# Kernel tuning notes

Hardware: AMD Instinct MI355X
Metric: run time of the kernel (lower is better)

Reference implementation:

```python
import jax, jax.numpy as jnp
import numpy as np

T, D, DFF, E, K, CAP = 8192, 1024, 4096, 8, 2, 2560


def setup_inputs() -> dict:
    key = jax.random.key(0)
    ks = jax.random.split(key, 6)
    return {
        "x_flat": jax.random.normal(ks[0], (T, D), dtype=jnp.float32),
        "idx_flat": jax.random.randint(ks[1], (T, K), 0, E, dtype=jnp.int32),
        "scores_flat": jax.random.uniform(ks[2], (T, K), dtype=jnp.float32),
        "capacity": CAP,
        "W1": jax.random.normal(ks[3], (E, D, DFF), dtype=jnp.float32) * 0.02,
        "B1": jnp.zeros((E, DFF), dtype=jnp.float32),
        "W2": jax.random.normal(ks[4], (E, DFF, D), dtype=jnp.float32) * 0.02,
        "B2": jnp.zeros((E, D), dtype=jnp.float32),
    }


def reference(x_flat, idx_flat, scores_flat, capacity, W1, B1, W2, B2):
    # Fused MoE dispatch: capacity-limited gather -> per-expert FFN (grouped GEMM)
    # -> weighted scatter-combine.
    Ttok, d = x_flat.shape
    k = idx_flat.shape[1]
    e = idx_flat.reshape(-1)                      # [T*k] expert id per assignment
    s = scores_flat.reshape(-1)                   # [T*k] gate score
    tok = jnp.repeat(jnp.arange(Ttok), k)         # [T*k] source token index

    oh = jax.nn.one_hot(e, W1.shape[0], dtype=jnp.int32)   # [T*k, E]
    # slot of each assignment within its expert (0-based arrival order)
    pos = jnp.sum(jnp.cumsum(oh, axis=0) * oh, axis=1) - 1  # [T*k]
    keep = pos < capacity                                   # drop overflow tokens
    pos_c = jnp.where(keep, pos, 0)

    # gather tokens into per-expert buffers [E, capacity, d]
    xe = jnp.zeros((W1.shape[0], capacity, d), dtype=x_flat.dtype)
    xe = xe.at[e, pos_c].add(jnp.where(keep[:, None], x_flat[tok], 0.0))

    # per-expert FFN (grouped GEMM)
    h = jax.nn.gelu(jnp.einsum('ecd,edf->ecf', xe, W1) + B1[:, None, :])
    y = jnp.einsum('ecf,efd->ecd', h, W2) + B2[:, None, :]   # [E, capacity, d]

    # scatter back, scaled by gate scores
    yg = y[e, pos_c] * (s * keep.astype(s.dtype))[:, None]   # [T*k, d]
    out = jnp.zeros_like(x_flat).at[tok].add(yg)
    return out
```

## Files before the change

kernel.cpp:

```cpp
#include <hip/hip_runtime.h>
#include <hip/hip_bf16.h>

#define T_TOK   8192
#define D_MODEL 1024
#define DFF     4096
#define N_EXP   8
#define TOPK    2
#define CAP     2560
#define NASSIGN (T_TOK * TOPK)

typedef unsigned short u16;
typedef __attribute__((ext_vector_type(8))) short  short8;
typedef __attribute__((ext_vector_type(8))) unsigned short u16x8;
typedef __attribute__((ext_vector_type(4))) float  f32x4;


__device__ inline u16 f2bf(float f) {
    union { float f; unsigned u; } v; v.f = f;
    unsigned u = v.u;
    unsigned r = (u + 0x7fffu + ((u >> 16) & 1u)) >> 16;
    return (u16)r;
}

__device__ inline float gelu_tanh(float x) {
    float z = 0.7978845608028654f * (x + 0.044715f * x * x * x);
    z = fminf(fmaxf(z, -15.f), 15.f);
    float ez = __expf(2.f * z);
    float t = (ez - 1.f) / (ez + 1.f);
    return 0.5f * x * (1.f + t);
}

__device__ inline void gload_lds16(const void* g, void* l) {
    __builtin_amdgcn_global_load_lds(
        (const __attribute__((address_space(1))) unsigned int*)g,
        (__attribute__((address_space(3))) unsigned int*)l, 16, 0, 0);
}

__global__ __launch_bounds__(256) void scan_kernel(
    const int* __restrict__ idx, int* __restrict__ counts,
    int* __restrict__ pos_arr, int* __restrict__ slot_src)
{
    const int eb = blockIdx.x;
    const int tid = threadIdx.x;
    __shared__ int sbuf[256];
    const int CHUNK = NASSIGN / 256;
    const int base_i = tid * CHUNK;
    int local = 0;
    #pragma unroll 8
    for (int j = 0; j < CHUNK; ++j) local += (idx[base_i + j] == eb) ? 1 : 0;
    sbuf[tid] = local;
    __syncthreads();
    for (int off = 1; off < 256; off <<= 1) {
        int v = (tid >= off) ? sbuf[tid - off] : 0;
        __syncthreads();
        sbuf[tid] += v;
        __syncthreads();
    }
    int run = sbuf[tid] - local;
    for (int j = 0; j < CHUNK; ++j) {
        int i = base_i + j;
        if (idx[i] == eb) {
            if (run < CAP) { pos_arr[i] = run; slot_src[eb * CAP + run] = i / TOPK; }
            else           { pos_arr[i] = -1; }
            ++run;
        }
    }
    if (tid == 0) {
        int tot = sbuf[255];
        counts[eb] = tot < CAP ? tot : CAP;
    }
}

__global__ __launch_bounds__(256) void transpose_cvt(
    const float* __restrict__ in, u16* __restrict__ out, int R, int C)
{
    __shared__ float tile[32][33];
    const int e = blockIdx.z;
    const int c0 = blockIdx.x * 32, r0 = blockIdx.y * 32;
    const float* ine = in + (size_t)e * R * C;
    u16* oute = out + (size_t)e * R * C;
    const int tx = threadIdx.x, ty = threadIdx.y;
    #pragma unroll
    for (int i = 0; i < 4; ++i) {
        int r = ty + i * 8;
        tile[r][tx] = ine[(size_t)(r0 + r) * C + c0 + tx];
    }
    __syncthreads();
    #pragma unroll
    for (int i = 0; i < 4; ++i) {
        int cr = ty + i * 8;
        oute[(size_t)(c0 + cr) * R + r0 + tx] = f2bf(tile[tx][cr]);
    }
}

__global__ __launch_bounds__(128) void gather_kernel(
    const float* __restrict__ x, const int* __restrict__ counts,
    const int* __restrict__ slot_src, u16* __restrict__ Xe)
{
    const int b = blockIdx.x;
    const int e = b / CAP, slot = b % CAP;
    const int tid = threadIdx.x;
    u16* dst = Xe + ((size_t)e * CAP + slot) * D_MODEL + tid * 8;
    if (slot < counts[e]) {
        const int tok = slot_src[b];
        const float4* src = (const float4*)(x + (size_t)tok * D_MODEL) + tid * 2;
        float4 a = src[0], c = src[1];
        u16x8 v;
        v[0] = f2bf(a.x); v[1] = f2bf(a.y); v[2] = f2bf(a.z); v[3] = f2bf(a.w);
        v[4] = f2bf(c.x); v[5] = f2bf(c.y); v[6] = f2bf(c.z); v[7] = f2bf(c.w);
        *(u16x8*)dst = v;
    } else {
        float4 z = {0.f, 0.f, 0.f, 0.f};
        *(float4*)dst = z;
    }
}

template<int KD, int ND, bool FUSE_GELU>
__global__ __launch_bounds__(256) void gemm_bt(
    const u16* __restrict__ A, const u16* __restrict__ Bt,
    const float* __restrict__ bias, void* __restrict__ Cout,
    const int* __restrict__ counts)
{
    const int e = blockIdx.z;
    const int brow = blockIdx.x * 128;
    if (brow >= counts[e]) return;
    const int bcol = blockIdx.y * 128;

    const char* Ae = (const char*)(A + (size_t)e * CAP * KD + (size_t)brow * KD);
    const char* Be = (const char*)(Bt + (size_t)e * ND * KD + (size_t)bcol * KD);

    __shared__ __align__(16) u16 lsA[128 * 32];
    __shared__ __align__(16) u16 lsB[128 * 32];

    const int tid = threadIdx.x;
    const int lane = tid & 63;
    const int w = tid >> 6;
    const int wr = (w >> 1) * 64, wc = (w & 1) * 64;
    const int lr = lane & 15, lq = lane >> 4;

    f32x4 acc[4][4] = {};

    const size_t rstride = (size_t)KD * 2;
    const char* ga0 = Ae + (size_t)(tid >> 2) * rstride + (size_t)(tid & 3) * 16;
    const char* gb0 = Be + (size_t)(tid >> 2) * rstride + (size_t)(tid & 3) * 16;
    char* la = (char*)lsA + tid * 16;
    char* lb = (char*)lsB + tid * 16;
    const size_t half = 64 * rstride;

    for (int kt = 0; kt < KD / 32; ++kt) {
        const size_t ko = (size_t)kt * 64;
        gload_lds16(ga0 + ko,        la);
        gload_lds16(ga0 + ko + half, la + 4096);
        gload_lds16(gb0 + ko,        lb);
        gload_lds16(gb0 + ko + half, lb + 4096);
        __syncthreads();
        short8 af[4], bfr[4];
        #pragma unroll
        for (int m = 0; m < 4; ++m)
            af[m] = *(const short8*)((const char*)lsA + ((wr + m * 16 + lr) * 64 + lq * 16));
        #pragma unroll
        for (int n = 0; n < 4; ++n)
            bfr[n] = *(const short8*)((const char*)lsB + ((wc + n * 16 + lr) * 64 + lq * 16));
        #pragma unroll
        for (int m = 0; m < 4; ++m)
            #pragma unroll
            for (int n = 0; n < 4; ++n)
                acc[m][n] = __builtin_amdgcn_mfma_f32_16x16x32_bf16(af[m], bfr[n], acc[m][n], 0, 0, 0);
        __syncthreads();
    }

    const float* be = bias + (size_t)e * ND + bcol;
    if (FUSE_GELU) {
        u16* Ce = (u16*)Cout + (size_t)e * CAP * ND + (size_t)brow * ND + bcol;
        #pragma unroll
        for (int m = 0; m < 4; ++m)
            #pragma unroll
            for (int n = 0; n < 4; ++n) {
                f32x4 v = acc[m][n];
                int c = wc + n * 16 + lr;
                float bb = be[c];
                #pragma unroll
                for (int j = 0; j < 4; ++j) {
                    int r = wr + m * 16 + lq * 4 + j;
                    Ce[(size_t)r * ND + c] = f2bf(gelu_tanh(v[j] + bb));
                }
            }
    } else {
        float* Ce = (float*)Cout + (size_t)e * CAP * ND + (size_t)brow * ND + bcol;
        #pragma unroll
        for (int m = 0; m < 4; ++m)
            #pragma unroll
            for (int n = 0; n < 4; ++n) {
                f32x4 v = acc[m][n];
                int c = wc + n * 16 + lr;
                float bb = be[c];
                #pragma unroll
                for (int j = 0; j < 4; ++j) {
                    int r = wr + m * 16 + lq * 4 + j;
                    Ce[(size_t)r * ND + c] = v[j] + bb;
                }
            }
    }
}

__global__ __launch_bounds__(256) void scatter_kernel(
    const int* __restrict__ idx, const float* __restrict__ scores,
    const int* __restrict__ pos_arr, const float* __restrict__ Y,
    float* __restrict__ out)
{
    const int t = blockIdx.x;
    const int tid = threadIdx.x;
    float4 acc = {0.f, 0.f, 0.f, 0.f};
    #pragma unroll
    for (int k = 0; k < TOPK; ++k) {
        int i = t * TOPK + k;
        int p = pos_arr[i];
        if (p >= 0) {
            int e = idx[i];
            float s = scores[i];
            float4 v = *(const float4*)(Y + ((size_t)e * CAP + p) * D_MODEL + tid * 4);
            acc.x += s * v.x; acc.y += s * v.y; acc.z += s * v.z; acc.w += s * v.w;
        }
    }
    *(float4*)(out + (size_t)t * D_MODEL + tid * 4) = acc;
}

extern "C" void kernel_launch(void* const* d_in, const int* in_sizes, int n_in,
                              void* d_out, int out_size, void* d_ws, size_t ws_size,
                              hipStream_t stream)
{
    const float* x      = (const float*)d_in[0];
    const int*   idx    = (const int*)d_in[1];
    const float* scores = (const float*)d_in[2];
    const float* W1 = (const float*)d_in[4];
    const float* B1 = (const float*)d_in[5];
    const float* W2 = (const float*)d_in[6];
    const float* B2 = (const float*)d_in[7];
    float* out = (float*)d_out;

    char* ws = (char*)d_ws;
    size_t off = 0;
    auto alloc = [&](size_t bytes) {
        char* p = ws + off;
        off += (bytes + 255) & ~(size_t)255;
        return p;
    };
    int* counts   = (int*)alloc(N_EXP * 4);
    int* pos_arr  = (int*)alloc((size_t)NASSIGN * 4);
    int* slot_src = (int*)alloc((size_t)N_EXP * CAP * 4);
    u16* W1b = (u16*)alloc((size_t)N_EXP * D_MODEL * DFF * 2);
    u16* Xe  = (u16*)alloc((size_t)N_EXP * CAP * D_MODEL * 2);
    u16* W2b = (u16*)alloc((size_t)N_EXP * DFF * D_MODEL * 2);
    u16* H   = (u16*)alloc((size_t)N_EXP * CAP * DFF * 2);
    float* Y = (float*)W1b;

    scan_kernel<<<N_EXP, 256, 0, stream>>>(idx, counts, pos_arr, slot_src);
    transpose_cvt<<<dim3(DFF / 32, D_MODEL / 32, N_EXP), dim3(32, 8), 0, stream>>>(
        W1, W1b, D_MODEL, DFF);
    transpose_cvt<<<dim3(D_MODEL / 32, DFF / 32, N_EXP), dim3(32, 8), 0, stream>>>(
        W2, W2b, DFF, D_MODEL);
    gather_kernel<<<N_EXP * CAP, 128, 0, stream>>>(x, counts, slot_src, Xe);
    gemm_bt<D_MODEL, DFF, true><<<dim3(CAP / 128, DFF / 128, N_EXP), 256, 0, stream>>>(
        Xe, W1b, B1, H, counts);
    gemm_bt<DFF, D_MODEL, false><<<dim3(CAP / 128, D_MODEL / 128, N_EXP), 256, 0, stream>>>(
        H, W2b, B2, Y, counts);
    scatter_kernel<<<T_TOK, 256, 0, stream>>>(idx, scores, pos_arr, Y, out);
}
```

Baseline: 830.1 us.

## Rewrite grouped GEMM as 256x256 tile, 8-wave, double-buffered swizzled LDS pipeline

Replaces the 128x128 single-buffered bf16 GEMM with a 256x256-tile, 512-thread kernel. It stages 64-wide K slices into 128KB of double-buffered LDS using XOR-swizzled async global-to-LDS loads, and interleaves prefetch of the next slices with MFMA groups under explicit barriers and vmcnt waits. It also remaps the flattened block id so neighbouring blocks are spread across XCDs, and it raises MFMA priority. The aim is to hide memory latency, cut LDS bank conflicts and raise arithmetic intensity, at the cost of large LDS use, high register pressure and hand-tuned waitcnt logic.

```diff
diff --git a/kernel.cpp b/kernel.cpp
--- a/kernel.cpp
+++ b/kernel.cpp
@@ -34,6 +34,14 @@
     __builtin_amdgcn_global_load_lds(
         (const __attribute__((address_space(1))) unsigned int*)g,
         (__attribute__((address_space(3))) unsigned int*)l, 16, 0, 0);
+}
+
+__device__ __forceinline__ void BARm() {
+    asm volatile("" ::: "memory");
+    __builtin_amdgcn_sched_barrier(0);
+    __builtin_amdgcn_s_barrier();
+    __builtin_amdgcn_sched_barrier(0);
+    asm volatile("" ::: "memory");
 }
 
 __global__ __launch_bounds__(256) void scan_kernel(
@@ -116,91 +124,146 @@
 }
 
 template<int KD, int ND, bool FUSE_GELU>
-__global__ __launch_bounds__(256) void gemm_bt(
+__global__ __launch_bounds__(512, 2) void gemm8(
     const u16* __restrict__ A, const u16* __restrict__ Bt,
     const float* __restrict__ bias, void* __restrict__ Cout,
-    const int* __restrict__ counts)
-{
-    const int e = blockIdx.z;
-    const int brow = blockIdx.x * 128;
+    const int* __restrict__ counts, int nx, int ny)
+{
+    __shared__ __align__(16) char lds[131072];
+
+    const int nwg = nx * ny * N_EXP;
+    const int cpx = nwg >> 3;
+    const int id2 = (blockIdx.x & 7) * cpx + (blockIdx.x >> 3);
+    const int e   = id2 / (nx * ny);
+    const int rem = id2 % (nx * ny);
+    const int bx = rem % nx, by = rem / nx;
+    const int brow = bx << 8;
     if (brow >= counts[e]) return;
-    const int bcol = blockIdx.y * 128;
-
-    const char* Ae = (const char*)(A + (size_t)e * CAP * KD + (size_t)brow * KD);
-    const char* Be = (const char*)(Bt + (size_t)e * ND * KD + (size_t)bcol * KD);
-
-    __shared__ __align__(16) u16 lsA[128 * 32];
-    __shared__ __align__(16) u16 lsB[128 * 32];
+    const int bcol = by << 8;
 
     const int tid = threadIdx.x;
+    const char* Ae = (const char*)(A + ((size_t)e * CAP + brow) * KD);
+    const char* Be = (const char*)(Bt + ((size_t)e * ND + bcol) * KD);
+    constexpr int RB = KD * 2;
+    constexpr int NT = KD / 64;
+
     const int lane = tid & 63;
-    const int w = tid >> 6;
-    const int wr = (w >> 1) * 64, wc = (w & 1) * 64;
+    const int wid = tid >> 6;
+    const int wm = wid >> 2, wn = wid & 3;
     const int lr = lane & 15, lq = lane >> 4;
 
-    f32x4 acc[4][4] = {};
-
-    const size_t rstride = (size_t)KD * 2;
-    const char* ga0 = Ae + (size_t)(tid >> 2) * rstride + (size_t)(tid & 3) * 16;
-    const char* gb0 = Be + (size_t)(tid >> 2) * rstride + (size_t)(tid & 3) * 16;
-    char* la = (char*)lsA + tid * 16;
-    char* lb = (char*)lsB + tid * 16;
-    const size_t half = 64 * rstride;
-
-    for (int kt = 0; kt < KD / 32; ++kt) {
-        const size_t ko = (size_t)kt * 64;
-        gload_lds16(ga0 + ko,        la);
-        gload_lds16(ga0 + ko + half, la + 4096);
-        gload_lds16(gb0 + ko,        lb);
-        gload_lds16(gb0 + ko + half, lb + 4096);
-        __syncthreads();
-        short8 af[4], bfr[4];
-        #pragma unroll
-        for (int m = 0; m < 4; ++m)
-            af[m] = *(const short8*)((const char*)lsA + ((wr + m * 16 + lr) * 64 + lq * 16));
-        #pragma unroll
-        for (int n = 0; n < 4; ++n)
-            bfr[n] = *(const short8*)((const char*)lsB + ((wc + n * 16 + lr) * 64 + lq * 16));
-        #pragma unroll
-        for (int m = 0; m < 4; ++m)
-            #pragma unroll
-            for (int n = 0; n < 4; ++n)
-                acc[m][n] = __builtin_amdgcn_mfma_f32_16x16x32_bf16(af[m], bfr[n], acc[m][n], 0, 0, 0);
-        __syncthreads();
+    const int srow0 = tid >> 2, ss = tid & 3;
+
+    #define STG(gbase, buf, slot, kb) do {                                         \
+        { int row_ = srow0;       int sl_ = ss ^ ((row_ >> 1) & 3);                \
+          gload_lds16((gbase) + (size_t)row_ * RB + (kb) + sl_ * 16,               \
+                      lds + (buf) * 65536 + (slot) * 16384 + tid * 16); }          \
+        { int row_ = 128 + srow0; int sl_ = ss ^ ((row_ >> 1) & 3);                \
+          gload_lds16((gbase) + (size_t)row_ * RB + (kb) + sl_ * 16,               \
+                      lds + (buf) * 65536 + (slot) * 16384 + 8192 + tid * 16); }   \
+    } while (0)
+
+    auto RD = [&](int buf, int slot, int row) -> short8 {
+        int sl = lq ^ ((row >> 1) & 3);
+        return *(const short8*)(lds + buf * 65536 + slot * 16384 + row * 64 + sl * 16);
+    };
+
+    f32x4 acc[8][4] = {};
+    short8 af[4], bf[4];
+
+    #define MFMA16(MB) do {                                                        \
+        __builtin_amdgcn_s_setprio(1);                                             \
+        _Pragma("unroll")                                                          \
+        for (int m_ = 0; m_ < 4; ++m_)                                             \
+            _Pragma("unroll")                                                      \
+            for (int n_ = 0; n_ < 4; ++n_)                                         \
+                acc[(MB) + m_][n_] = __builtin_amdgcn_mfma_f32_16x16x32_bf16(      \
+                    af[m_], bf[n_], acc[(MB) + m_][n_], 0, 0, 0);                  \
+        __builtin_amdgcn_s_setprio(0);                                             \
+    } while (0)
+
+    STG(Ae, 0, 0, 0);
+    STG(Be, 0, 2, 0);
+    STG(Ae, 0, 1, 64);
+    STG(Be, 0, 3, 64);
+    STG(Ae, 1, 0, 128);
+    STG(Be, 1, 2, 128);
+    asm volatile("s_waitcnt vmcnt(4)" ::: "memory");
+    BARm();
+
+    for (int t = 0; t < NT; ++t) {
+        const int buf = t & 1;
+        const int obuf = buf ^ 1;
+
+        #pragma unroll
+        for (int n = 0; n < 4; ++n) bf[n] = RD(buf, 2, wn * 64 + n * 16 + lr);
+        #pragma unroll
+        for (int m = 0; m < 4; ++m) af[m] = RD(buf, 0, wm * 128 + m * 16 + lr);
+        if (t + 1 < NT) STG(Ae, obuf, 1, (t + 1) * 128 + 64);
+        BARm();
+        MFMA16(0);
+        BARm();
+
+        #pragma unroll
+        for (int m = 0; m < 4; ++m) af[m] = RD(buf, 0, wm * 128 + (4 + m) * 16 + lr);
+        if (t + 1 < NT) STG(Be, obuf, 3, (t + 1) * 128 + 64);
+        BARm();
+        MFMA16(4);
+        BARm();
+
+        #pragma unroll
+        for (int n = 0; n < 4; ++n) bf[n] = RD(buf, 3, wn * 64 + n * 16 + lr);
+        #pragma unroll
+        for (int m = 0; m < 4; ++m) af[m] = RD(buf, 1, wm * 128 + m * 16 + lr);
+        if (t + 2 < NT) STG(Ae, buf, 0, (t + 2) * 128);
+        BARm();
+        MFMA16(0);
+        BARm();
+
+        #pragma unroll
+        for (int m = 0; m < 4; ++m) af[m] = RD(buf, 1, wm * 128 + (4 + m) * 16 + lr);
+        if (t + 2 < NT) STG(Be, buf, 2, (t + 2) * 128);
+        BARm();
+        MFMA16(4);
+        if (t + 2 < NT)      { asm volatile("s_waitcnt vmcnt(4)" ::: "memory"); }
+        else if (t + 1 < NT) { asm volatile("s_waitcnt vmcnt(0)" ::: "memory"); }
+        BARm();
     }
 
     const float* be = bias + (size_t)e * ND + bcol;
     if (FUSE_GELU) {
-        u16* Ce = (u16*)Cout + (size_t)e * CAP * ND + (size_t)brow * ND + bcol;
-        #pragma unroll
-        for (int m = 0; m < 4; ++m)
+        u16* Ce = (u16*)Cout + ((size_t)e * CAP + brow) * ND + bcol;
+        #pragma unroll
+        for (int m = 0; m < 8; ++m)
             #pragma unroll
             for (int n = 0; n < 4; ++n) {
                 f32x4 v = acc[m][n];
-                int c = wc + n * 16 + lr;
+                int c = wn * 64 + n * 16 + lr;
                 float bb = be[c];
                 #pragma unroll
                 for (int j = 0; j < 4; ++j) {
-                    int r = wr + m * 16 + lq * 4 + j;
+                    int r = wm * 128 + m * 16 + lq * 4 + j;
                     Ce[(size_t)r * ND + c] = f2bf(gelu_tanh(v[j] + bb));
                 }
             }
     } else {
-        float* Ce = (float*)Cout + (size_t)e * CAP * ND + (size_t)brow * ND + bcol;
-        #pragma unroll
-        for (int m = 0; m < 4; ++m)
+        float* Ce = (float*)Cout + ((size_t)e * CAP + brow) * ND + bcol;
+        #pragma unroll
+        for (int m = 0; m < 8; ++m)
             #pragma unroll
             for (int n = 0; n < 4; ++n) {
                 f32x4 v = acc[m][n];
-                int c = wc + n * 16 + lr;
+                int c = wn * 64 + n * 16 + lr;
                 float bb = be[c];
                 #pragma unroll
                 for (int j = 0; j < 4; ++j) {
-                    int r = wr + m * 16 + lq * 4 + j;
+                    int r = wm * 128 + m * 16 + lq * 4 + j;
                     Ce[(size_t)r * ND + c] = v[j] + bb;
                 }
             }
     }
+    #undef STG
+    #undef MFMA16
 }
 
 __global__ __launch_bounds__(256) void scatter_kernel(
@@ -260,9 +323,9 @@
     transpose_cvt<<<dim3(D_MODEL / 32, DFF / 32, N_EXP), dim3(32, 8), 0, stream>>>(
         W2, W2b, DFF, D_MODEL);
     gather_kernel<<<N_EXP * CAP, 128, 0, stream>>>(x, counts, slot_src, Xe);
-    gemm_bt<D_MODEL, DFF, true><<<dim3(CAP / 128, DFF / 128, N_EXP), 256, 0, stream>>>(
-        Xe, W1b, B1, H, counts);
-    gemm_bt<DFF, D_MODEL, false><<<dim3(CAP / 128, D_MODEL / 128, N_EXP), 256, 0, stream>>>(
-        H, W2b, B2, Y, counts);
+    gemm8<D_MODEL, DFF, true><<<(CAP / 256) * (DFF / 256) * N_EXP, 512, 0, stream>>>(
+        Xe, W1b, B1, H, counts, CAP / 256, DFF / 256);
+    gemm8<DFF, D_MODEL, false><<<(CAP / 256) * (D_MODEL / 256) * N_EXP, 512, 0, stream>>>(
+        H, W2b, B2, Y, counts, CAP / 256, D_MODEL / 256);
     scatter_kernel<<<T_TOK, 256, 0, stream>>>(idx, scores, pos_arr, Y, out);
 }
```

New measurement: 795.7 us. -4.1%, faster.
